# Kernel tuning notes

Hardware: AMD Instinct MI355X
Metric: run time of the kernel (lower is better)

Reference implementation:

```python
import jax, jax.numpy as jnp
import numpy as np

NUM_HEADS = 16
D_K = 8  # == n_qubits


def setup_inputs() -> dict:
    key = jax.random.key(0)
    k1, k2, k3 = jax.random.split(key, 3)
    x = jax.random.normal(k1, (4, 2048, 128), dtype=jnp.float32)
    # trainable RX angles, one per qubit (tq.RX has_params=True)
    theta = jax.random.normal(k2, (D_K,), dtype=jnp.float32)
    # out_proj: Linear(embed_dim, embed_dim, bias=False)
    w_out = jax.random.normal(k3, (128, 128), dtype=jnp.float32) * (1.0 / np.sqrt(128.0))
    return {"x": x, "theta": theta, "w_out": w_out}


def quantum_features(x, theta):
    # x: [b, s, e]. Per head of size d_k: encode RX(x_i), trainable RX(theta_i)
    # (composes to RX(x_i + theta_i)), CNOT ladder [i, i+1], measure PauliZ.
    # Heisenberg picture: Z_w -> Z_0...Z_w, so <Z_w> = prod_{i<=w} cos(x_i + theta_i).
    b, s, e = x.shape
    heads = x.reshape(b, s, NUM_HEADS, D_K)
    return jnp.cumprod(jnp.cos(heads + theta), axis=-1)  # [b, s, h, d_k]


def reference(x, theta, w_out):
    b, s, e = x.shape
    # q == k == v: same shared q_layer applied to the same x three times.
    qkv = quantum_features(x, theta)            # [b, s, h, d_k]
    q = qkv.transpose(0, 2, 1, 3)               # [b, h, s, d_k]
    scores = jnp.einsum('bhqd,bhkd->bhqk', q, q) / np.sqrt(D_K)
    attn = jax.nn.softmax(scores, axis=-1)      # dropout is identity at eval
    out = jnp.einsum('bhqk,bhkd->bhqd', attn, q)
    out = out.transpose(0, 2, 1, 3).reshape(b, s, e)
    return out @ w_out.T
```

## Files before the change

kernel.cpp:

```cpp
#include <hip/hip_runtime.h>

#define BATCH 4
#define SEQ   2048
#define EMB   128
#define NH    16
#define DK    8

#define QSCALE 0.510069726f

typedef _Float16 v4h  __attribute__((ext_vector_type(4)));
typedef _Float16 v8h  __attribute__((ext_vector_type(8)));
typedef __fp16   v2fp __attribute__((ext_vector_type(2)));
typedef float    v4f  __attribute__((ext_vector_type(4)));
typedef float    v16f __attribute__((ext_vector_type(16)));

#define CHUNK  512
#define NCH    (SEQ / CHUNK)
#define VTP    520

__launch_bounds__(256, 4)
__global__ void attn_kernel(const float* __restrict__ x,
                            const float* __restrict__ theta,
                            _Float16* __restrict__ Ah ) {
  __shared__ __align__(16) _Float16 Kl[CHUNK * 8];
  __shared__ __align__(16) _Float16 VT[10][VTP];

  const int tid = threadIdx.x;
  const int L   = tid & 63;
  const int ln  = L & 31;
  const int hf  = L >> 5;
  const int wv  = tid >> 6;
  const int bh     = blockIdx.x >> 4;
  const int qchunk = blockIdx.x & 15;
  const int qb     = qchunk * 128 + wv * 32;
  const int b = bh >> 4;
  const int h = bh & 15;

  float th[DK];
#pragma unroll
  for (int i = 0; i < DK; ++i) th[i] = theta[i];

  for (int i = tid; i < VTP; i += 256) {
    VT[8][i] = (_Float16)1.0f;
    VT[9][i] = (_Float16)0.0f;
  }

  const int c0 = qchunk >> 2;
  const int mrow = (ln < 9) ? ln : 9;
  const float* xb = x + (size_t)b * SEQ * EMB + h * DK;

  float4 pa0, pa1, pb0, pb1;
  {
    const float* xp = xb + (size_t)(c0 * CHUNK + tid) * EMB;
    pa0 = *(const float4*)(xp);
    pa1 = *(const float4*)(xp + 4);
    pb0 = *(const float4*)(xp + 256 * EMB);
    pb1 = *(const float4*)(xp + 256 * EMB + 4);
  }

  v8h qf = {0, 0, 0, 0, 0, 0, 0, 0};
  v16f acc;
#pragma unroll
  for (int i = 0; i < 16; ++i) acc[i] = 0.f;
  v16f zf;
#pragma unroll
  for (int i = 0; i < 16; ++i) zf[i] = 0.f;

  for (int cc = 0; cc < NCH; ++cc) {
    if (cc) __syncthreads();

    {
      float r0[8], r1[8];
      r0[0] = __cosf(pa0.x + th[0]);
      r0[1] = r0[0] * __cosf(pa0.y + th[1]);
      r0[2] = r0[1] * __cosf(pa0.z + th[2]);
      r0[3] = r0[2] * __cosf(pa0.w + th[3]);
      r0[4] = r0[3] * __cosf(pa1.x + th[4]);
      r0[5] = r0[4] * __cosf(pa1.y + th[5]);
      r0[6] = r0[5] * __cosf(pa1.z + th[6]);
      r0[7] = r0[6] * __cosf(pa1.w + th[7]);
      r1[0] = __cosf(pb0.x + th[0]);
      r1[1] = r1[0] * __cosf(pb0.y + th[1]);
      r1[2] = r1[1] * __cosf(pb0.z + th[2]);
      r1[3] = r1[2] * __cosf(pb0.w + th[3]);
      r1[4] = r1[3] * __cosf(pb1.x + th[4]);
      r1[5] = r1[4] * __cosf(pb1.y + th[5]);
      r1[6] = r1[5] * __cosf(pb1.z + th[6]);
      r1[7] = r1[6] * __cosf(pb1.w + th[7]);

      _Float16 h0[8], h1[8];
#pragma unroll
      for (int i = 0; i < 8; ++i) { h0[i] = (_Float16)r0[i]; h1[i] = (_Float16)r1[i]; }

      union { v4h v[2]; float4 f; } u0, u1;
      u0.v[0] = (v4h){h0[0], h0[1], h0[2], h0[3]};
      u0.v[1] = (v4h){h0[4], h0[5], h0[6], h0[7]};
      u1.v[0] = (v4h){h1[0], h1[1], h1[2], h1[3]};
      u1.v[1] = (v4h){h1[4], h1[5], h1[6], h1[7]};
      *(float4*)&Kl[tid * 8]         = u0.f;
      *(float4*)&Kl[(tid + 256) * 8] = u1.f;

      const int j0 = tid, j1 = tid + 256;
      const int col0 = (j0 & ~15) | (j0 & 3) | ((j0 & 4) << 1) | ((j0 & 8) >> 1);
      const int col1 = (j1 & ~15) | (j1 & 3) | ((j1 & 4) << 1) | ((j1 & 8) >> 1);
#pragma unroll
      for (int d = 0; d < 8; ++d) {
        VT[d][col0] = h0[d];
        VT[d][col1] = h1[d];
      }
    }
    __syncthreads();

    if (cc + 1 < NCH) {
      const int cn = (c0 + cc + 1) & (NCH - 1);
      const float* xp = xb + (size_t)(cn * CHUNK + tid) * EMB;
      pa0 = *(const float4*)(xp);
      pa1 = *(const float4*)(xp + 4);
      pb0 = *(const float4*)(xp + 256 * EMB);
      pb1 = *(const float4*)(xp + 256 * EMB + 4);
    }

    if (cc == 0 && hf == 0) {
      const int ql = (qchunk & 3) * 128 + wv * 32 + ln;
      v8h qv = *(const v8h*)&Kl[ql * 8];
      const _Float16 qs = (_Float16)QSCALE;
      const v8h qsc = {qs, qs, qs, qs, qs, qs, qs, qs};
      qf = qv * qsc;
    }

    v8h kf_a = *(const v8h*)&Kl[ln * 8];
    v16f s_cur = __builtin_amdgcn_mfma_f32_32x32x16_f16(kf_a, qf, zf, 0, 0, 0);
    kf_a = *(const v8h*)&Kl[(32 + ln) * 8];

#pragma unroll 5
    for (int kb = 0; kb < 15; ++kb) {
      const v8h kf_b = *(const v8h*)&Kl[((((kb + 2) & 15) * 32) + ln) * 8];
      const v16f s_next = __builtin_amdgcn_mfma_f32_32x32x16_f16(kf_a, qf, zf, 0, 0, 0);
      const v8h vt0 = *(const v8h*)&VT[mrow][kb * 32 + hf * 8];
      const v8h vt1 = *(const v8h*)&VT[mrow][kb * 32 + 16 + hf * 8];
      union { v2fp p[4]; v8h v; } p0, p1;
#pragma unroll
      for (int i = 0; i < 4; ++i) {
        p0.p[i] = __builtin_amdgcn_cvt_pkrtz(
            __builtin_amdgcn_exp2f(s_cur[2 * i]),
            __builtin_amdgcn_exp2f(s_cur[2 * i + 1]));
      }
      acc = __builtin_amdgcn_mfma_f32_32x32x16_f16(vt0, p0.v, acc, 0, 0, 0);
#pragma unroll
      for (int i = 0; i < 4; ++i) {
        p1.p[i] = __builtin_amdgcn_cvt_pkrtz(
            __builtin_amdgcn_exp2f(s_cur[8 + 2 * i]),
            __builtin_amdgcn_exp2f(s_cur[8 + 2 * i + 1]));
      }
      acc = __builtin_amdgcn_mfma_f32_32x32x16_f16(vt1, p1.v, acc, 0, 0, 0);
      s_cur = s_next;
      kf_a  = kf_b;
    }
    {
      const int kb = 15;
      const v8h vt0 = *(const v8h*)&VT[mrow][kb * 32 + hf * 8];
      const v8h vt1 = *(const v8h*)&VT[mrow][kb * 32 + 16 + hf * 8];
      union { v2fp p[4]; v8h v; } p0, p1;
#pragma unroll
      for (int i = 0; i < 4; ++i) {
        p0.p[i] = __builtin_amdgcn_cvt_pkrtz(
            __builtin_amdgcn_exp2f(s_cur[2 * i]),
            __builtin_amdgcn_exp2f(s_cur[2 * i + 1]));
        p1.p[i] = __builtin_amdgcn_cvt_pkrtz(
            __builtin_amdgcn_exp2f(s_cur[8 + 2 * i]),
            __builtin_amdgcn_exp2f(s_cur[8 + 2 * i + 1]));
      }
      acc = __builtin_amdgcn_mfma_f32_32x32x16_f16(vt0, p0.v, acc, 0, 0, 0);
      acc = __builtin_amdgcn_mfma_f32_32x32x16_f16(vt1, p1.v, acc, 0, 0, 0);
    }
  }

  {
    const float den = __shfl(acc[4], ln, 64);
    const float inv = 1.0f / den;
    const int qrow = qb + ln;
    v4h o = {(_Float16)(acc[0] * inv), (_Float16)(acc[1] * inv),
             (_Float16)(acc[2] * inv), (_Float16)(acc[3] * inv)};
    *(v4h*)(Ah + ((size_t)b * SEQ + qrow) * EMB + h * DK + hf * 4) = o;
  }
}

__launch_bounds__(256, 4)
__global__ void proj_kernel(const _Float16* __restrict__ Ah,
                            const float* __restrict__ W,
                            float* __restrict__ out) {
  __shared__ __align__(16) _Float16 Ahs[64][136];
  __shared__ __align__(16) _Float16 Whs[64][136];

  const int tid  = threadIdx.x;
  const int L    = tid & 63;
  const int wv   = tid >> 6;
  const int quad = L >> 4;
  const int ln   = L & 15;
  const int rowbase = blockIdx.x * 64;
  const int colbase = blockIdx.y * 64;

#pragma unroll
  for (int it = 0; it < 4; ++it) {
    const int idx = it * 256 + tid;
    const int r  = idx >> 4;
    const int c8 = idx & 15;
    *(uint4*)&Ahs[r][c8 * 8] =
        *(const uint4*)(Ah + (size_t)(rowbase + r) * EMB + c8 * 8);
  }
#pragma unroll
  for (int it = 0; it < 8; ++it) {
    const int idx = it * 256 + tid;
    const int n  = idx >> 5;
    const int c4 = idx & 31;
    const float4 w = *(const float4*)(W + (size_t)(colbase + n) * EMB + c4 * 4);
    v4h wh = {(_Float16)w.x, (_Float16)w.y, (_Float16)w.z, (_Float16)w.w};
    *(v4h*)&Whs[n][c4 * 4] = wh;
  }
  __syncthreads();

  v4f acc[4];
#pragma unroll
  for (int nt = 0; nt < 4; ++nt) acc[nt] = (v4f){0.f, 0.f, 0.f, 0.f};

#pragma unroll
  for (int k8 = 0; k8 < 8; ++k8) {
    const v4h af = *(const v4h*)&Ahs[wv * 16 + ln][k8 * 16 + quad * 4];
#pragma unroll
    for (int nt = 0; nt < 4; ++nt) {
      const v4h bf = *(const v4h*)&Whs[nt * 16 + ln][k8 * 16 + quad * 4];
      acc[nt] = __builtin_amdgcn_mfma_f32_16x16x16f16(af, bf, acc[nt], 0, 0, 0);
    }
  }

#pragma unroll
  for (int nt = 0; nt < 4; ++nt) {
    const int col = colbase + nt * 16 + ln;
#pragma unroll
    for (int r = 0; r < 4; ++r) {
      out[(size_t)(rowbase + wv * 16 + quad * 4 + r) * EMB + col] = acc[nt][r];
    }
  }
}

extern "C" void kernel_launch(void* const* d_in, const int* in_sizes, int n_in,
                              void* d_out, int out_size, void* d_ws, size_t ws_size,
                              hipStream_t stream) {
  const float* x     = (const float*)d_in[0];
  const float* theta = (const float*)d_in[1];
  const float* w_out = (const float*)d_in[2];
  float* out = (float*)d_out;

  _Float16* Ah = (_Float16*)d_ws;

  attn_kernel<<<dim3(1024), dim3(256), 0, stream>>>(x, theta, Ah);

  proj_kernel<<<dim3((BATCH * SEQ) / 64, 2), dim3(256), 0, stream>>>(Ah, w_out, out);
}
```

Baseline: 94.00 us.

## Precompute quantum features in separate kernel and stream K/V from global memory

Splits feature computation into a new feat_kernel that writes fp16 K rows and a permuted transposed V buffer (with a ones row for the softmax denominator) to workspace. The attention kernel then reads K and V fragments straight from global/L2 with register prefetching, with no LDS staging and no per-chunk __syncthreads. This removes the redundant cosine recomputation done by every query block and the barrier stalls. In exchange it adds a kernel launch, a workspace round-trip, and global-memory latency in the inner loop.

```diff
diff --git a/kernel.cpp b/kernel.cpp
--- a/kernel.cpp
+++ b/kernel.cpp
@@ -14,51 +14,77 @@
 typedef float    v4f  __attribute__((ext_vector_type(4)));
 typedef float    v16f __attribute__((ext_vector_type(16)));
 
-#define CHUNK  512
-#define NCH    (SEQ / CHUNK)
-#define VTP    520
 
 __launch_bounds__(256, 4)
-__global__ void attn_kernel(const float* __restrict__ x,
+__global__ void feat_kernel(const float* __restrict__ x,
                             const float* __restrict__ theta,
+                            _Float16* __restrict__ F1,
+                            _Float16* __restrict__ F2) {
+  const int tid = threadIdx.x;
+  const int bh  = blockIdx.x >> 3;
+  const int s   = ((blockIdx.x & 7) << 8) + tid;
+  const int b = bh >> 4, h = bh & 15;
+
+  float th[8];
+#pragma unroll
+  for (int i = 0; i < 8; ++i) th[i] = theta[i];
+
+  const float* xp = x + ((size_t)b * SEQ + s) * EMB + h * DK;
+  const float4 a = *(const float4*)(xp);
+  const float4 c = *(const float4*)(xp + 4);
+  float r[8];
+  r[0] = __cosf(a.x + th[0]);
+  r[1] = r[0] * __cosf(a.y + th[1]);
+  r[2] = r[1] * __cosf(a.z + th[2]);
+  r[3] = r[2] * __cosf(a.w + th[3]);
+  r[4] = r[3] * __cosf(c.x + th[4]);
+  r[5] = r[4] * __cosf(c.y + th[5]);
+  r[6] = r[5] * __cosf(c.z + th[6]);
+  r[7] = r[6] * __cosf(c.w + th[7]);
+
+  _Float16 hv[8];
+#pragma unroll
+  for (int i = 0; i < 8; ++i) hv[i] = (_Float16)r[i];
+
+  union { v4h v[2]; float4 f; } u;
+  u.v[0] = (v4h){hv[0], hv[1], hv[2], hv[3]};
+  u.v[1] = (v4h){hv[4], hv[5], hv[6], hv[7]};
+  *(float4*)(F1 + ((size_t)bh * SEQ + s) * 8) = u.f;
+
+  const int sp = (s & ~15) | (s & 3) | ((s & 4) << 1) | ((s & 8) >> 1);
+  _Float16* f2 = F2 + (size_t)bh * 9 * SEQ;
+#pragma unroll
+  for (int d = 0; d < 8; ++d) f2[(size_t)d * SEQ + sp] = hv[d];
+  f2[(size_t)8 * SEQ + s] = (_Float16)1.0f;
+}
+
+__launch_bounds__(256, 4)
+__global__ void attn_kernel(const _Float16* __restrict__ F1,
+                            const _Float16* __restrict__ F2,
                             _Float16* __restrict__ Ah ) {
-  __shared__ __align__(16) _Float16 Kl[CHUNK * 8];
-  __shared__ __align__(16) _Float16 VT[10][VTP];
-
   const int tid = threadIdx.x;
   const int L   = tid & 63;
   const int ln  = L & 31;
   const int hf  = L >> 5;
   const int wv  = tid >> 6;
-  const int bh     = blockIdx.x >> 4;
-  const int qchunk = blockIdx.x & 15;
-  const int qb     = qchunk * 128 + wv * 32;
-  const int b = bh >> 4;
-  const int h = bh & 15;
-
-  float th[DK];
-#pragma unroll
-  for (int i = 0; i < DK; ++i) th[i] = theta[i];
-
-  for (int i = tid; i < VTP; i += 256) {
-    VT[8][i] = (_Float16)1.0f;
-    VT[9][i] = (_Float16)0.0f;
-  }
-
-  const int c0 = qchunk >> 2;
-  const int mrow = (ln < 9) ? ln : 9;
-  const float* xb = x + (size_t)b * SEQ * EMB + h * DK;
-
-  float4 pa0, pa1, pb0, pb1;
-  {
-    const float* xp = xb + (size_t)(c0 * CHUNK + tid) * EMB;
-    pa0 = *(const float4*)(xp);
-    pa1 = *(const float4*)(xp + 4);
-    pb0 = *(const float4*)(xp + 256 * EMB);
-    pb1 = *(const float4*)(xp + 256 * EMB + 4);
-  }
+  const int bh  = blockIdx.x >> 4;
+  const int qt  = (blockIdx.x & 15) * 4 + wv;
+  const int qb  = qt * 32;
+  const int b = bh >> 4, h = bh & 15;
+  const int mrow = (ln < 8) ? ln : 8;
+
+  const _Float16* f1 = F1 + (size_t)bh * SEQ * 8;
+  const _Float16* kp = f1 + ln * 8;
+  const _Float16* vp = F2 + (size_t)bh * 9 * SEQ + (size_t)mrow * SEQ + hf * 8;
 
   v8h qf = {0, 0, 0, 0, 0, 0, 0, 0};
+  if (hf == 0) {
+    const v8h qv = *(const v8h*)(f1 + (size_t)(qb + ln) * 8);
+    const _Float16 qs = (_Float16)QSCALE;
+    const v8h qsc = {qs, qs, qs, qs, qs, qs, qs, qs};
+    qf = qv * qsc;
+  }
+
   v16f acc;
 #pragma unroll
   for (int i = 0; i < 16; ++i) acc[i] = 0.f;
@@ -66,113 +92,48 @@
 #pragma unroll
   for (int i = 0; i < 16; ++i) zf[i] = 0.f;
 
-  for (int cc = 0; cc < NCH; ++cc) {
-    if (cc) __syncthreads();
-
-    {
-      float r0[8], r1[8];
-      r0[0] = __cosf(pa0.x + th[0]);
-      r0[1] = r0[0] * __cosf(pa0.y + th[1]);
-      r0[2] = r0[1] * __cosf(pa0.z + th[2]);
-      r0[3] = r0[2] * __cosf(pa0.w + th[3]);
-      r0[4] = r0[3] * __cosf(pa1.x + th[4]);
-      r0[5] = r0[4] * __cosf(pa1.y + th[5]);
-      r0[6] = r0[5] * __cosf(pa1.z + th[6]);
-      r0[7] = r0[6] * __cosf(pa1.w + th[7]);
-      r1[0] = __cosf(pb0.x + th[0]);
-      r1[1] = r1[0] * __cosf(pb0.y + th[1]);
-      r1[2] = r1[1] * __cosf(pb0.z + th[2]);
-      r1[3] = r1[2] * __cosf(pb0.w + th[3]);
-      r1[4] = r1[3] * __cosf(pb1.x + th[4]);
-      r1[5] = r1[4] * __cosf(pb1.y + th[5]);
-      r1[6] = r1[5] * __cosf(pb1.z + th[6]);
-      r1[7] = r1[6] * __cosf(pb1.w + th[7]);
-
-      _Float16 h0[8], h1[8];
-#pragma unroll
-      for (int i = 0; i < 8; ++i) { h0[i] = (_Float16)r0[i]; h1[i] = (_Float16)r1[i]; }
-
-      union { v4h v[2]; float4 f; } u0, u1;
-      u0.v[0] = (v4h){h0[0], h0[1], h0[2], h0[3]};
-      u0.v[1] = (v4h){h0[4], h0[5], h0[6], h0[7]};
-      u1.v[0] = (v4h){h1[0], h1[1], h1[2], h1[3]};
-      u1.v[1] = (v4h){h1[4], h1[5], h1[6], h1[7]};
-      *(float4*)&Kl[tid * 8]         = u0.f;
-      *(float4*)&Kl[(tid + 256) * 8] = u1.f;
-
-      const int j0 = tid, j1 = tid + 256;
-      const int col0 = (j0 & ~15) | (j0 & 3) | ((j0 & 4) << 1) | ((j0 & 8) >> 1);
-      const int col1 = (j1 & ~15) | (j1 & 3) | ((j1 & 4) << 1) | ((j1 & 8) >> 1);
-#pragma unroll
-      for (int d = 0; d < 8; ++d) {
-        VT[d][col0] = h0[d];
-        VT[d][col1] = h1[d];
-      }
-    }
-    __syncthreads();
-
-    if (cc + 1 < NCH) {
-      const int cn = (c0 + cc + 1) & (NCH - 1);
-      const float* xp = xb + (size_t)(cn * CHUNK + tid) * EMB;
-      pa0 = *(const float4*)(xp);
-      pa1 = *(const float4*)(xp + 4);
-      pb0 = *(const float4*)(xp + 256 * EMB);
-      pb1 = *(const float4*)(xp + 256 * EMB + 4);
-    }
-
-    if (cc == 0 && hf == 0) {
-      const int ql = (qchunk & 3) * 128 + wv * 32 + ln;
-      v8h qv = *(const v8h*)&Kl[ql * 8];
-      const _Float16 qs = (_Float16)QSCALE;
-      const v8h qsc = {qs, qs, qs, qs, qs, qs, qs, qs};
-      qf = qv * qsc;
-    }
-
-    v8h kf_a = *(const v8h*)&Kl[ln * 8];
-    v16f s_cur = __builtin_amdgcn_mfma_f32_32x32x16_f16(kf_a, qf, zf, 0, 0, 0);
-    kf_a = *(const v8h*)&Kl[(32 + ln) * 8];
-
-#pragma unroll 5
-    for (int kb = 0; kb < 15; ++kb) {
-      const v8h kf_b = *(const v8h*)&Kl[((((kb + 2) & 15) * 32) + ln) * 8];
-      const v16f s_next = __builtin_amdgcn_mfma_f32_32x32x16_f16(kf_a, qf, zf, 0, 0, 0);
-      const v8h vt0 = *(const v8h*)&VT[mrow][kb * 32 + hf * 8];
-      const v8h vt1 = *(const v8h*)&VT[mrow][kb * 32 + 16 + hf * 8];
-      union { v2fp p[4]; v8h v; } p0, p1;
-#pragma unroll
-      for (int i = 0; i < 4; ++i) {
-        p0.p[i] = __builtin_amdgcn_cvt_pkrtz(
-            __builtin_amdgcn_exp2f(s_cur[2 * i]),
-            __builtin_amdgcn_exp2f(s_cur[2 * i + 1]));
-      }
-      acc = __builtin_amdgcn_mfma_f32_32x32x16_f16(vt0, p0.v, acc, 0, 0, 0);
-#pragma unroll
-      for (int i = 0; i < 4; ++i) {
-        p1.p[i] = __builtin_amdgcn_cvt_pkrtz(
-            __builtin_amdgcn_exp2f(s_cur[8 + 2 * i]),
-            __builtin_amdgcn_exp2f(s_cur[8 + 2 * i + 1]));
-      }
-      acc = __builtin_amdgcn_mfma_f32_32x32x16_f16(vt1, p1.v, acc, 0, 0, 0);
-      s_cur = s_next;
-      kf_a  = kf_b;
-    }
-    {
-      const int kb = 15;
-      const v8h vt0 = *(const v8h*)&VT[mrow][kb * 32 + hf * 8];
-      const v8h vt1 = *(const v8h*)&VT[mrow][kb * 32 + 16 + hf * 8];
-      union { v2fp p[4]; v8h v; } p0, p1;
-#pragma unroll
-      for (int i = 0; i < 4; ++i) {
-        p0.p[i] = __builtin_amdgcn_cvt_pkrtz(
-            __builtin_amdgcn_exp2f(s_cur[2 * i]),
-            __builtin_amdgcn_exp2f(s_cur[2 * i + 1]));
-        p1.p[i] = __builtin_amdgcn_cvt_pkrtz(
-            __builtin_amdgcn_exp2f(s_cur[8 + 2 * i]),
-            __builtin_amdgcn_exp2f(s_cur[8 + 2 * i + 1]));
-      }
-      acc = __builtin_amdgcn_mfma_f32_32x32x16_f16(vt0, p0.v, acc, 0, 0, 0);
-      acc = __builtin_amdgcn_mfma_f32_32x32x16_f16(vt1, p1.v, acc, 0, 0, 0);
-    }
+  v8h kf0  = *(const v8h*)kp; kp += 256;
+  v8h kf_n = *(const v8h*)kp; kp += 256;
+  v8h vt0_c = *(const v8h*)(vp);
+  v8h vt1_c = *(const v8h*)(vp + 16); vp += 32;
+  v16f s_cur = __builtin_amdgcn_mfma_f32_32x32x16_f16(kf0, qf, zf, 0, 0, 0);
+
+#pragma unroll 4
+  for (int kb = 0; kb < 63; ++kb) {
+    const v8h kf_f = *(const v8h*)kp; kp += 256;
+    const v16f s_next = __builtin_amdgcn_mfma_f32_32x32x16_f16(kf_n, qf, zf, 0, 0, 0);
+    const v8h vt0_n = *(const v8h*)(vp);
+    const v8h vt1_n = *(const v8h*)(vp + 16); vp += 32;
+    union { v2fp p[4]; v8h v; } p0, p1;
+#pragma unroll
+    for (int i = 0; i < 4; ++i) {
+      p0.p[i] = __builtin_amdgcn_cvt_pkrtz(
+          __builtin_amdgcn_exp2f(s_cur[2 * i]),
+          __builtin_amdgcn_exp2f(s_cur[2 * i + 1]));
+    }
+    acc = __builtin_amdgcn_mfma_f32_32x32x16_f16(vt0_c, p0.v, acc, 0, 0, 0);
+#pragma unroll
+    for (int i = 0; i < 4; ++i) {
+      p1.p[i] = __builtin_amdgcn_cvt_pkrtz(
+          __builtin_amdgcn_exp2f(s_cur[8 + 2 * i]),
+          __builtin_amdgcn_exp2f(s_cur[8 + 2 * i + 1]));
+    }
+    acc = __builtin_amdgcn_mfma_f32_32x32x16_f16(vt1_c, p1.v, acc, 0, 0, 0);
+    s_cur = s_next; kf_n = kf_f; vt0_c = vt0_n; vt1_c = vt1_n;
+  }
+  {
+    union { v2fp p[4]; v8h v; } p0, p1;
+#pragma unroll
+    for (int i = 0; i < 4; ++i) {
+      p0.p[i] = __builtin_amdgcn_cvt_pkrtz(
+          __builtin_amdgcn_exp2f(s_cur[2 * i]),
+          __builtin_amdgcn_exp2f(s_cur[2 * i + 1]));
+      p1.p[i] = __builtin_amdgcn_cvt_pkrtz(
+          __builtin_amdgcn_exp2f(s_cur[8 + 2 * i]),
+          __builtin_amdgcn_exp2f(s_cur[8 + 2 * i + 1]));
+    }
+    acc = __builtin_amdgcn_mfma_f32_32x32x16_f16(vt0_c, p0.v, acc, 0, 0, 0);
+    acc = __builtin_amdgcn_mfma_f32_32x32x16_f16(vt1_c, p1.v, acc, 0, 0, 0);
   }
 
   {
@@ -252,8 +213,12 @@
   float* out = (float*)d_out;
 
   _Float16* Ah = (_Float16*)d_ws;
-
-  attn_kernel<<<dim3(1024), dim3(256), 0, stream>>>(x, theta, Ah);
+  _Float16* F1 = Ah + (size_t)BATCH * SEQ * EMB;
+  _Float16* F2 = F1 + (size_t)64 * SEQ * 8 + 512;
+
+  feat_kernel<<<dim3(512), dim3(256), 0, stream>>>(x, theta, F1, F2);
+
+  attn_kernel<<<dim3(1024), dim3(256), 0, stream>>>(F1, F2, Ah);
 
   proj_kernel<<<dim3((BATCH * SEQ) / 64, 2), dim3(256), 0, stream>>>(Ah, w_out, out);
 }
```

Result: slower. 100.6 us (+7.0%).
